# Kernel optimization log

Measured on AMD Instinct MI355X. Metric: run time of the kernel, lower is better.

## Reference

```python
import jax, jax.numpy as jnp
import numpy as np

B = 8388608
NUM_CLASSES = 3
ALPHA = 0.25
GAMMA = 2.0
CRIT_PENALTY = 50.0
PENALTY = np.array([[0.0, 2.0, 5.0], [8.0, 0.0, 3.0], [50.0, 20.0, 0.0]], dtype=np.float32)


def setup_inputs() -> dict:
    key = jax.random.key(0)
    k1, k2 = jax.random.split(key)
    outputs = jax.random.normal(k1, (B, NUM_CLASSES), dtype=jnp.float32)
    targets = jax.random.randint(k2, (B,), 0, NUM_CLASSES, dtype=jnp.int64)
    class_weights = jnp.array([1.0, 2.0, 5.0], dtype=jnp.float32)
    penalty_matrix = jnp.asarray(PENALTY)
    return {"outputs": outputs, "targets": targets,
            "class_weights": class_weights, "penalty_matrix": penalty_matrix}


def reference(outputs, targets, class_weights, penalty_matrix):
    # log-softmax once; per-sample CE
    log_p = jax.nn.log_softmax(outputs, axis=1)                     # [B, C]
    ce_raw = -jnp.take_along_axis(log_p, targets[:, None], axis=1)[:, 0]  # [B]

    # weighted CE with mean reduction (torch: sum(w_t * ce) / sum(w_t))
    w_t = class_weights[targets]                                    # [B]
    ce_loss = jnp.sum(w_t * ce_raw) / jnp.sum(w_t)

    # focal component
    pt = jnp.exp(-ce_raw)
    focal_loss = jnp.mean(ALPHA * (1.0 - pt) ** GAMMA * ce_raw)

    # safety penalty: vectorized gather penalty_matrix[true, pred]
    pred_classes = jnp.argmax(outputs, axis=1)                      # [B]
    safety_penalty = jnp.mean(penalty_matrix[targets, pred_classes])

    # critical-miss penalty (class 2)
    critical_mask = targets == 2
    n_crit = jnp.sum(critical_mask)
    misses = jnp.sum(critical_mask & (pred_classes != 2)).astype(jnp.float32)
    critical_penalty = jnp.where(
        n_crit > 0,
        misses / jnp.maximum(n_crit, 1).astype(jnp.float32) * CRIT_PENALTY,
        0.0,
    )

    total = ce_loss + 0.3 * focal_loss + 0.4 * safety_penalty + 0.6 * critical_penalty
    return total
```

## Files before the change

### kernel.cpp

```cpp
#include <hip/hip_runtime.h>


#define THREADS 256
#define SAMPLES 8
#define SPB (THREADS * SAMPLES)

__global__ __launch_bounds__(THREADS) void loss_main(
    const float* __restrict__ outp,
    const int*   __restrict__ tgt,
    const float* __restrict__ cw,
    const float* __restrict__ pen,
    float*       __restrict__ partial,
    int n, int nblocks)
{
    __shared__ float4 lut[9];
    const int tid = threadIdx.x;
    if (tid < 9) {
        int t = (tid >= 6) ? 2 : ((tid >= 3) ? 1 : 0);
        int p = tid - t * 3;
        float4 e;
        e.x = pen[tid];
        e.y = cw[t];
        e.z = (t == 1) ? 4096.f : ((t == 2) ? 1.f : 0.f);
        e.w = (t == 2 && p != 2) ? 1.f : 0.f;
        lut[tid] = e;
    }
    __syncthreads();

    float s_wce = 0.f, s_f = 0.f, s_s = 0.f, s_cnt = 0.f, s_miss = 0.f;

    const long long base = ((long long)blockIdx.x * THREADS + tid) * SAMPLES;

    if (base + SAMPLES - 1 < n) {
        const float4* o4 = (const float4*)(outp + base * 3);
        const int4*   t4 = (const int4*)(tgt + base);
        float xf[3 * SAMPLES];
        *(float4*)&xf[ 0] = o4[0]; *(float4*)&xf[ 4] = o4[1]; *(float4*)&xf[ 8] = o4[2];
        *(float4*)&xf[12] = o4[3]; *(float4*)&xf[16] = o4[4]; *(float4*)&xf[20] = o4[5];
        int ti[SAMPLES];
        *(int4*)&ti[0] = t4[0]; *(int4*)&ti[4] = t4[1];

#pragma unroll
        for (int k = 0; k < SAMPLES; ++k) {
            float x0 = xf[3*k+0], x1 = xf[3*k+1], x2 = xf[3*k+2];
            int t = ti[k];
            float e0 = __expf(x0);
            float e1 = __expf(x1);
            float e2 = __expf(x2);
            float s  = e0 + e1 + e2;
            bool  t0 = (t == 0), t1 = (t == 1);
            float xt = t0 ? x0 : (t1 ? x1 : x2);
            float et = t0 ? e0 : (t1 ? e1 : e2);
            float ce = __logf(s) - xt;
            float pt = __fdividef(et, s);
            bool  g10 = (x1 > x0);
            int   pred = g10 ? 1 : 0;
            float xp   = g10 ? x1 : x0;
            if (x2 > xp) pred = 2;

            float4 L = lut[t * 3 + pred];
            s_s   += L.x;
            s_wce += L.y * ce;
            float om = 1.f - pt;
            s_f   += om * om * ce;
            s_cnt += L.z;
            s_miss+= L.w;
        }
    } else {
        for (int k = 0; k < SAMPLES; ++k) {
            long long i = base + k;
            if (i >= n) break;
            float x0 = outp[i*3+0], x1 = outp[i*3+1], x2 = outp[i*3+2];
            int t = tgt[i];
            float e0 = __expf(x0), e1 = __expf(x1), e2 = __expf(x2);
            float s  = e0 + e1 + e2;
            bool  t0 = (t == 0), t1 = (t == 1);
            float xt = t0 ? x0 : (t1 ? x1 : x2);
            float et = t0 ? e0 : (t1 ? e1 : e2);
            float ce = __logf(s) - xt;
            float pt = __fdividef(et, s);
            bool  g10 = (x1 > x0);
            int   pred = g10 ? 1 : 0;
            float xp   = g10 ? x1 : x0;
            if (x2 > xp) pred = 2;
            float4 L = lut[t * 3 + pred];
            s_s   += L.x;
            s_wce += L.y * ce;
            float om = 1.f - pt;
            s_f   += om * om * ce;
            s_cnt += L.z;
            s_miss+= L.w;
        }
    }

#pragma unroll
    for (int off = 32; off > 0; off >>= 1) {
        s_wce  += __shfl_down(s_wce,  off);
        s_f    += __shfl_down(s_f,    off);
        s_s    += __shfl_down(s_s,    off);
        s_cnt  += __shfl_down(s_cnt,  off);
        s_miss += __shfl_down(s_miss, off);
    }

    __shared__ float fred[4][5];
    const int lane = tid & 63;
    const int wave = tid >> 6;
    if (lane == 0) {
        fred[wave][0] = s_wce; fred[wave][1] = s_f;  fred[wave][2] = s_s;
        fred[wave][3] = s_cnt; fred[wave][4] = s_miss;
    }
    __syncthreads();
    if (tid < 5) {
        float v = fred[0][tid] + fred[1][tid] + fred[2][tid] + fred[3][tid];
        partial[tid * nblocks + blockIdx.x] = v;
    }
}

__global__ __launch_bounds__(256) void loss_finalize(
    const float* __restrict__ partial,
    float* __restrict__ out, int nblocks, int n)
{
    double a_wce = 0, a_f = 0, a_s = 0, a_n1 = 0, a_n2 = 0, a_miss = 0;
    for (int i = threadIdx.x; i < nblocks; i += 256) {
        a_wce += (double)partial[0 * nblocks + i];
        a_f   += (double)partial[1 * nblocks + i];
        a_s   += (double)partial[2 * nblocks + i];
        float c  = partial[3 * nblocks + i];
        float n1 = floorf(c * (1.f / 4096.f));
        a_n1 += (double)n1;
        a_n2 += (double)(c - n1 * 4096.f);
        a_miss += (double)partial[4 * nblocks + i];
    }
    double acc[6] = {a_wce, a_f, a_s, a_n1, a_n2, a_miss};
#pragma unroll
    for (int off = 32; off > 0; off >>= 1) {
#pragma unroll
        for (int j = 0; j < 6; ++j)
            acc[j] += __shfl_down(acc[j], off);
    }
    __shared__ double dred[4][6];
    const int lane = threadIdx.x & 63;
    const int wave = threadIdx.x >> 6;
    if (lane == 0) {
#pragma unroll
        for (int j = 0; j < 6; ++j) dred[wave][j] = acc[j];
    }
    __syncthreads();
    if (threadIdx.x == 0) {
        double t[6];
#pragma unroll
        for (int j = 0; j < 6; ++j)
            t[j] = dred[0][j] + dred[1][j] + dred[2][j] + dred[3][j];
        double n1 = t[3], n2 = t[4];
        double s_w = (double)n + n1 + 4.0 * n2;
        double inv_b   = 1.0 / (double)n;
        double ce_loss = t[0] / s_w;
        double focal   = 0.25 * t[1] * inv_b;
        double safety  = t[2] * inv_b;
        double crit    = (n2 > 0.0) ? (t[5] / n2 * 50.0) : 0.0;
        out[0] = (float)(ce_loss + 0.3 * focal + 0.4 * safety + 0.6 * crit);
    }
}

extern "C" void kernel_launch(void* const* d_in, const int* in_sizes, int n_in,
                              void* d_out, int out_size, void* d_ws, size_t ws_size,
                              hipStream_t stream) {
    const float* outp = (const float*)d_in[0];
    const int*   tgt  = (const int*)d_in[1];
    const float* cw   = (const float*)d_in[2];
    const float* pen  = (const float*)d_in[3];
    float* out = (float*)d_out;
    const int n = in_sizes[1];

    const int nblocks = (n + SPB - 1) / SPB;
    float* partial = (float*)d_ws;

    loss_main<<<nblocks, THREADS, 0, stream>>>(outp, tgt, cw, pen, partial, n, nblocks);
    loss_finalize<<<1, 256, 0, stream>>>(partial, out, nblocks, n);
}
```

Before: 179.8 us.

## Issue two chunks of loads per thread upfront and replace LDS LUT with register selects

Each thread now handles two 8-sample chunks and issues all global loads for both chunks before any compute, with a sched_barrier so the loads stay grouped. This raises memory-level parallelism and halves the block count. The shared-memory lookup table and its __syncthreads are replaced by scalar loads of the class weights and penalty matrix plus select chains. The cost is higher register pressure and more ALU selects per sample.

New measurement: 181.5 us. Within noise of the previous version (+1.0%).

```diff
diff --git a/kernel.cpp b/kernel.cpp
--- a/kernel.cpp
+++ b/kernel.cpp
@@ -2,8 +2,9 @@
 
 
 #define THREADS 256
-#define SAMPLES 8
-#define SPB (THREADS * SAMPLES)
+#define CHUNK 8
+#define NCHUNK 2
+#define SPB (THREADS * CHUNK * NCHUNK)
 
 __global__ __launch_bounds__(THREADS) void loss_main(
     const float* __restrict__ outp,
@@ -13,83 +14,111 @@
     float*       __restrict__ partial,
     int n, int nblocks)
 {
-    __shared__ float4 lut[9];
+    const float cw0 = cw[0], cw1 = cw[1], cw2 = cw[2];
+    const float p00 = pen[0], p01 = pen[1], p02 = pen[2];
+    const float p10 = pen[3], p11 = pen[4], p12 = pen[5];
+    const float p20 = pen[6], p21 = pen[7], p22 = pen[8];
+
+    float s_wce = 0.f, s_f = 0.f, s_s = 0.f, s_cnt = 0.f, s_miss = 0.f;
+
     const int tid = threadIdx.x;
-    if (tid < 9) {
-        int t = (tid >= 6) ? 2 : ((tid >= 3) ? 1 : 0);
-        int p = tid - t * 3;
-        float4 e;
-        e.x = pen[tid];
-        e.y = cw[t];
-        e.z = (t == 1) ? 4096.f : ((t == 2) ? 1.f : 0.f);
-        e.w = (t == 2 && p != 2) ? 1.f : 0.f;
-        lut[tid] = e;
-    }
-    __syncthreads();
-
-    float s_wce = 0.f, s_f = 0.f, s_s = 0.f, s_cnt = 0.f, s_miss = 0.f;
-
-    const long long base = ((long long)blockIdx.x * THREADS + tid) * SAMPLES;
-
-    if (base + SAMPLES - 1 < n) {
-        const float4* o4 = (const float4*)(outp + base * 3);
-        const int4*   t4 = (const int4*)(tgt + base);
-        float xf[3 * SAMPLES];
-        *(float4*)&xf[ 0] = o4[0]; *(float4*)&xf[ 4] = o4[1]; *(float4*)&xf[ 8] = o4[2];
-        *(float4*)&xf[12] = o4[3]; *(float4*)&xf[16] = o4[4]; *(float4*)&xf[20] = o4[5];
-        int ti[SAMPLES];
-        *(int4*)&ti[0] = t4[0]; *(int4*)&ti[4] = t4[1];
-
-#pragma unroll
-        for (int k = 0; k < SAMPLES; ++k) {
-            float x0 = xf[3*k+0], x1 = xf[3*k+1], x2 = xf[3*k+2];
-            int t = ti[k];
-            float e0 = __expf(x0);
-            float e1 = __expf(x1);
-            float e2 = __expf(x2);
-            float s  = e0 + e1 + e2;
-            bool  t0 = (t == 0), t1 = (t == 1);
-            float xt = t0 ? x0 : (t1 ? x1 : x2);
-            float et = t0 ? e0 : (t1 ? e1 : e2);
-            float ce = __logf(s) - xt;
-            float pt = __fdividef(et, s);
-            bool  g10 = (x1 > x0);
-            int   pred = g10 ? 1 : 0;
-            float xp   = g10 ? x1 : x0;
-            if (x2 > xp) pred = 2;
-
-            float4 L = lut[t * 3 + pred];
-            s_s   += L.x;
-            s_wce += L.y * ce;
-            float om = 1.f - pt;
-            s_f   += om * om * ce;
-            s_cnt += L.z;
-            s_miss+= L.w;
+    const long long blk0 = (long long)blockIdx.x * SPB;
+    const bool full = (blk0 + SPB <= (long long)n);
+
+    if (full) {
+        float4 va[6]; int4 taA, tbA;
+        float4 vb[6]; int4 taB, tbB;
+
+        {
+            const long long base = blk0 + (long long)tid * CHUNK;
+            const float4* o4 = (const float4*)(outp + base * 3);
+            const int4*   t4 = (const int4*)(tgt + base);
+            va[0]=o4[0]; va[1]=o4[1]; va[2]=o4[2]; va[3]=o4[3]; va[4]=o4[4]; va[5]=o4[5];
+            taA=t4[0]; tbA=t4[1];
+        }
+        {
+            const long long base = blk0 + (long long)(THREADS * CHUNK) + (long long)tid * CHUNK;
+            const float4* o4 = (const float4*)(outp + base * 3);
+            const int4*   t4 = (const int4*)(tgt + base);
+            vb[0]=o4[0]; vb[1]=o4[1]; vb[2]=o4[2]; vb[3]=o4[3]; vb[4]=o4[4]; vb[5]=o4[5];
+            taB=t4[0]; tbB=t4[1];
+        }
+        __builtin_amdgcn_sched_barrier(0);
+
+#pragma unroll
+        for (int c = 0; c < NCHUNK; ++c) {
+            float xf[3 * CHUNK];
+            int   ti[CHUNK];
+            if (c == 0) {
+                *(float4*)&xf[ 0]=va[0]; *(float4*)&xf[ 4]=va[1]; *(float4*)&xf[ 8]=va[2];
+                *(float4*)&xf[12]=va[3]; *(float4*)&xf[16]=va[4]; *(float4*)&xf[20]=va[5];
+                *(int4*)&ti[0]=taA; *(int4*)&ti[4]=tbA;
+            } else {
+                *(float4*)&xf[ 0]=vb[0]; *(float4*)&xf[ 4]=vb[1]; *(float4*)&xf[ 8]=vb[2];
+                *(float4*)&xf[12]=vb[3]; *(float4*)&xf[16]=vb[4]; *(float4*)&xf[20]=vb[5];
+                *(int4*)&ti[0]=taB; *(int4*)&ti[4]=tbB;
+            }
+
+#pragma unroll
+            for (int k = 0; k < CHUNK; ++k) {
+                float x0 = xf[3*k+0], x1 = xf[3*k+1], x2 = xf[3*k+2];
+                int t = ti[k];
+                float e0 = __expf(x0);
+                float e1 = __expf(x1);
+                float e2 = __expf(x2);
+                float s  = e0 + e1 + e2;
+                bool  t0 = (t == 0), t1 = (t == 1);
+                float xt = t0 ? x0 : (t1 ? x1 : x2);
+                float et = t0 ? e0 : (t1 ? e1 : e2);
+                float ce = __logf(s) - xt;
+                float pt = __fdividef(et, s);
+                bool  g10 = (x1 > x0);
+                int   pred = g10 ? 1 : 0;
+                float xp   = g10 ? x1 : x0;
+                if (x2 > xp) pred = 2;
+
+                float w = t0 ? cw0 : (t1 ? cw1 : cw2);
+                s_wce += w * ce;
+                float om = 1.f - pt;
+                s_f   += om * om * ce;
+                float r0 = (pred == 0) ? p00 : ((pred == 1) ? p01 : p02);
+                float r1 = (pred == 0) ? p10 : ((pred == 1) ? p11 : p12);
+                float r2 = (pred == 0) ? p20 : ((pred == 1) ? p21 : p22);
+                s_s   += t0 ? r0 : (t1 ? r1 : r2);
+                s_cnt += t1 ? 4096.f : ((!t0) ? 1.f : 0.f);
+                s_miss+= (!t0 && !t1 && pred != 2) ? 1.f : 0.f;
+            }
         }
     } else {
-        for (int k = 0; k < SAMPLES; ++k) {
-            long long i = base + k;
-            if (i >= n) break;
-            float x0 = outp[i*3+0], x1 = outp[i*3+1], x2 = outp[i*3+2];
-            int t = tgt[i];
-            float e0 = __expf(x0), e1 = __expf(x1), e2 = __expf(x2);
-            float s  = e0 + e1 + e2;
-            bool  t0 = (t == 0), t1 = (t == 1);
-            float xt = t0 ? x0 : (t1 ? x1 : x2);
-            float et = t0 ? e0 : (t1 ? e1 : e2);
-            float ce = __logf(s) - xt;
-            float pt = __fdividef(et, s);
-            bool  g10 = (x1 > x0);
-            int   pred = g10 ? 1 : 0;
-            float xp   = g10 ? x1 : x0;
-            if (x2 > xp) pred = 2;
-            float4 L = lut[t * 3 + pred];
-            s_s   += L.x;
-            s_wce += L.y * ce;
-            float om = 1.f - pt;
-            s_f   += om * om * ce;
-            s_cnt += L.z;
-            s_miss+= L.w;
+        for (int c = 0; c < NCHUNK; ++c) {
+            for (int k = 0; k < CHUNK; ++k) {
+                long long i = blk0 + (long long)c * (THREADS * CHUNK)
+                            + (long long)tid * CHUNK + k;
+                if (i >= n) continue;
+                float x0 = outp[i*3+0], x1 = outp[i*3+1], x2 = outp[i*3+2];
+                int t = tgt[i];
+                float e0 = __expf(x0), e1 = __expf(x1), e2 = __expf(x2);
+                float s  = e0 + e1 + e2;
+                bool  t0 = (t == 0), t1 = (t == 1);
+                float xt = t0 ? x0 : (t1 ? x1 : x2);
+                float et = t0 ? e0 : (t1 ? e1 : e2);
+                float ce = __logf(s) - xt;
+                float pt = __fdividef(et, s);
+                bool  g10 = (x1 > x0);
+                int   pred = g10 ? 1 : 0;
+                float xp   = g10 ? x1 : x0;
+                if (x2 > xp) pred = 2;
+                float w = t0 ? cw0 : (t1 ? cw1 : cw2);
+                s_wce += w * ce;
+                float om = 1.f - pt;
+                s_f   += om * om * ce;
+                float r0 = (pred == 0) ? p00 : ((pred == 1) ? p01 : p02);
+                float r1 = (pred == 0) ? p10 : ((pred == 1) ? p11 : p12);
+                float r2 = (pred == 0) ? p20 : ((pred == 1) ? p21 : p22);
+                s_s   += t0 ? r0 : (t1 ? r1 : r2);
+                s_cnt += t1 ? 4096.f : ((!t0) ? 1.f : 0.f);
+                s_miss+= (!t0 && !t1 && pred != 2) ? 1.f : 0.f;
+            }
         }
     }
 
```
